# Optimization experiments

Measured on AMD Instinct MI355X. Metric: run time of the kernel, lower is better.

## Reference

```python
import jax, jax.numpy as jnp
import numpy as np

DIM = 1024
HEADS = 16
MLP = 4096
EPS = 1e-5

def _layer_norm(x, g, b):
    mu = jnp.mean(x, axis=-1, keepdims=True)
    var = jnp.mean(jnp.square(x - mu), axis=-1, keepdims=True)
    return (x - mu) * jax.lax.rsqrt(var + EPS) * g + b

def setup_inputs() -> dict:
    key = jax.random.key(0)
    ks = jax.random.split(key, 8)
    s = 0.02
    return {
        "x": jax.random.normal(ks[0], (2, 2048, DIM), dtype=jnp.float32),
        "ln1_g": jnp.ones((DIM,), jnp.float32),
        "ln1_b": jnp.zeros((DIM,), jnp.float32),
        "qkv_w": jax.random.normal(ks[1], (DIM, 3 * DIM), jnp.float32) * s,
        "qkv_b": jnp.zeros((3 * DIM,), jnp.float32),
        "proj_w": jax.random.normal(ks[2], (DIM, DIM), jnp.float32) * s,
        "proj_b": jnp.zeros((DIM,), jnp.float32),
        "ln2_g": jnp.ones((DIM,), jnp.float32),
        "ln2_b": jnp.zeros((DIM,), jnp.float32),
        "fc1_w": jax.random.normal(ks[3], (DIM, MLP), jnp.float32) * s,
        "fc1_b": jnp.zeros((MLP,), jnp.float32),
        "fc2_w": jax.random.normal(ks[4], (MLP, DIM), jnp.float32) * s,
        "fc2_b": jnp.zeros((DIM,), jnp.float32),
    }

def reference(x, ln1_g, ln1_b, qkv_w, qkv_b, proj_w, proj_b,
              ln2_g, ln2_b, fc1_w, fc1_b, fc2_w, fc2_b):
    B, N, C = x.shape
    H = HEADS
    D = C // H
    # --- attention (pre-norm); NOTE: source applies no 1/sqrt(D) scaling ---
    h = _layer_norm(x, ln1_g, ln1_b)
    qkv = (h @ qkv_w + qkv_b).reshape(B, N, 3, H, D)
    q, k, v = (qkv[:, :, 0], qkv[:, :, 1], qkv[:, :, 2])  # [B,N,H,D]
    qk = jnp.einsum('bnhd,bmhd->bhnm', q, k)
    attn = jax.nn.softmax(qk, axis=-1)
    y = jnp.einsum('bhnm,bmhd->bnhd', attn, v).reshape(B, N, C)
    y = y @ proj_w + proj_b
    x = x + y
    # --- MLP (pre-norm), exact GELU like torch nn.GELU ---
    h2 = _layer_norm(x, ln2_g, ln2_b)
    h2 = jax.nn.gelu(h2 @ fc1_w + fc1_b, approximate=False)
    x = x + (h2 @ fc2_w + fc2_b)
    return x
```

## Files before the change

### kernel.cpp

```cpp
#include <hip/hip_runtime.h>
#include <hip/hip_bf16.h>

#define CDIM   1024
#define NSEQ   2048
#define NHEAD  16
#define HDIM   64
#define MLPDIM 4096
#define TROWS  4096

typedef __attribute__((ext_vector_type(8)))  __bf16 bf16x8;
typedef __attribute__((ext_vector_type(4)))  float  f32x4;
typedef __attribute__((ext_vector_type(16))) float  f32x16;
typedef __attribute__((ext_vector_type(4)))  unsigned short us4;

static __device__ __forceinline__ unsigned short f2bf(float f) {
  unsigned int u = __float_as_uint(f);
  u += 0x7fffu + ((u >> 16) & 1u);
  return (unsigned short)(u >> 16);
}

#define MFMA16(a, b, c) __builtin_amdgcn_mfma_f32_16x16x32_bf16(a, b, c, 0, 0, 0)
#define MFMA32(a, b, c) __builtin_amdgcn_mfma_f32_32x32x16_bf16(a, b, c, 0, 0, 0)

static __device__ __forceinline__ void gll16(const unsigned short* g, unsigned short* l) {
  __builtin_amdgcn_global_load_lds(
      (const __attribute__((address_space(1))) unsigned int*)g,
      (__attribute__((address_space(3))) unsigned int*)l, 16, 0, 0);
}

__global__ __launch_bounds__(256)
void ln_bf16_kernel(const float* __restrict__ x,
                    const float* __restrict__ gam,
                    const float* __restrict__ bet,
                    unsigned short* __restrict__ out)
{
  int row = blockIdx.x;
  int t = threadIdx.x;
  const float4* xr = (const float4*)(x + (size_t)row * CDIM);
  float4 v = xr[t];
  float s  = v.x + v.y + v.z + v.w;
  float s2 = v.x*v.x + v.y*v.y + v.z*v.z + v.w*v.w;
  #pragma unroll
  for (int off = 32; off > 0; off >>= 1) {
    s  += __shfl_down(s, off);
    s2 += __shfl_down(s2, off);
  }
  __shared__ float rs[4], rs2[4];
  int wave = t >> 6, lane = t & 63;
  if (lane == 0) { rs[wave] = s; rs2[wave] = s2; }
  __syncthreads();
  float fs  = rs[0] + rs[1] + rs[2] + rs[3];
  float fs2 = rs2[0] + rs2[1] + rs2[2] + rs2[3];
  float mu   = fs * (1.0f / CDIM);
  float var  = fs2 * (1.0f / CDIM) - mu * mu;
  float rstd = rsqrtf(var + 1e-5f);
  float4 gg = ((const float4*)gam)[t];
  float4 bb = ((const float4*)bet)[t];
  us4 o;
  o.x = f2bf((v.x - mu) * rstd * gg.x + bb.x);
  o.y = f2bf((v.y - mu) * rstd * gg.y + bb.y);
  o.z = f2bf((v.z - mu) * rstd * gg.z + bb.z);
  o.w = f2bf((v.w - mu) * rstd * gg.w + bb.w);
  ((us4*)(out + (size_t)row * CDIM))[t] = o;
}

__global__ __launch_bounds__(256)
void ln_add_bf16_kernel(float* __restrict__ x, const float* __restrict__ pp,
                        const float* __restrict__ gam, const float* __restrict__ bet,
                        unsigned short* __restrict__ out)
{
  int row = blockIdx.x;
  int t = threadIdx.x;
  float4* xr = (float4*)(x + (size_t)row * CDIM);
  const float4* pr = (const float4*)(pp + (size_t)row * CDIM);
  float4 v = xr[t];
  float4 q = pr[t];
  v.x += q.x; v.y += q.y; v.z += q.z; v.w += q.w;
  xr[t] = v;
  float s  = v.x + v.y + v.z + v.w;
  float s2 = v.x*v.x + v.y*v.y + v.z*v.z + v.w*v.w;
  #pragma unroll
  for (int off = 32; off > 0; off >>= 1) {
    s  += __shfl_down(s, off);
    s2 += __shfl_down(s2, off);
  }
  __shared__ float rs[4], rs2[4];
  int wave = t >> 6, lane = t & 63;
  if (lane == 0) { rs[wave] = s; rs2[wave] = s2; }
  __syncthreads();
  float fs  = rs[0] + rs[1] + rs[2] + rs[3];
  float fs2 = rs2[0] + rs2[1] + rs2[2] + rs2[3];
  float mu   = fs * (1.0f / CDIM);
  float var  = fs2 * (1.0f / CDIM) - mu * mu;
  float rstd = rsqrtf(var + 1e-5f);
  float4 gg = ((const float4*)gam)[t];
  float4 bb = ((const float4*)bet)[t];
  us4 o;
  o.x = f2bf((v.x - mu) * rstd * gg.x + bb.x);
  o.y = f2bf((v.y - mu) * rstd * gg.y + bb.y);
  o.z = f2bf((v.z - mu) * rstd * gg.z + bb.z);
  o.w = f2bf((v.w - mu) * rstd * gg.w + bb.w);
  ((us4*)(out + (size_t)row * CDIM))[t] = o;
}

__global__ __launch_bounds__(256)
void wt_bf16_kernel(const float* __restrict__ W, unsigned short* __restrict__ Wt,
                    int K, int N)
{
  __shared__ float tile[32][33];
  int n0 = blockIdx.x * 32, k0 = blockIdx.y * 32;
  int t = threadIdx.x;
  int r = t >> 3, c4 = (t & 7) << 2;
  float4 v = *(const float4*)(W + (size_t)(k0 + r) * N + n0 + c4);
  tile[r][c4 + 0] = v.x; tile[r][c4 + 1] = v.y;
  tile[r][c4 + 2] = v.z; tile[r][c4 + 3] = v.w;
  __syncthreads();
  us4 o;
  o.x = f2bf(tile[c4 + 0][r]);
  o.y = f2bf(tile[c4 + 1][r]);
  o.z = f2bf(tile[c4 + 2][r]);
  o.w = f2bf(tile[c4 + 3][r]);
  *(us4*)(Wt + (size_t)(n0 + r) * K + k0 + c4) = o;
}

template<int EPI>
__global__ __launch_bounds__(256, 4)
void gemm_bt(const unsigned short* __restrict__ A, const unsigned short* __restrict__ Bt,
             const float* __restrict__ bias, int Kstride, int Kc, int nbx, int nby,
             float* __restrict__ outf, unsigned short* __restrict__ outb,
             const float* __restrict__ resid, float* __restrict__ pp,
             unsigned short* __restrict__ qo, unsigned short* __restrict__ ko,
             unsigned short* __restrict__ vo)
{
  __shared__ unsigned short As[2][128 * 32];
  __shared__ unsigned short Bs[2][128 * 32];
  const int tid  = threadIdx.x;
  const int lane = tid & 63;
  const int wave = tid >> 6;
  const int wr = wave >> 1, wc = wave & 1;
  const int g = lane >> 4, r16 = lane & 15;

  const int nwg = gridDim.x;
  const int orig = ((int)blockIdx.x & 7) * (nwg >> 3) + ((int)blockIdx.x >> 3);
  const int bx = orig % nbx;
  const int t2 = orig / nbx;
  const int by = t2 % nby;
  const int kz = t2 / nby;
  const int bm = by * 128, bn = bx * 128;
  const int kbase = kz * Kc;
  const int N = nbx * 128;

  auto stage = [&](int d, int k0) {
    #pragma unroll
    for (int c = 0; c < 2; c++) {
      int o   = (c * 256 + tid) << 3;
      int row = o >> 5;
      int col = o & 31;
      int ub  = (c * 256 + (tid & ~63)) << 3;
      gll16(A  + (size_t)(bm + row) * Kstride + kbase + k0 + col, &As[d][ub]);
      gll16(Bt + (size_t)(bn + row) * Kstride + kbase + k0 + col, &Bs[d][ub]);
    }
  };

  f32x4 acc[4][4];
  #pragma unroll
  for (int i = 0; i < 4; i++)
    #pragma unroll
    for (int j = 0; j < 4; j++) acc[i][j] = (f32x4){0.f, 0.f, 0.f, 0.f};

  stage(0, 0);
  const int nkt = Kc / 32;
  for (int kt = 0; kt < nkt; kt++) {
    const int cur = kt & 1;
    __syncthreads();
    if (kt + 1 < nkt) stage(cur ^ 1, (kt + 1) * 32);
    bf16x8 af[4], bfr[4];
    #pragma unroll
    for (int i = 0; i < 4; i++) {
      int row = wr * 64 + i * 16 + r16;
      af[i] = *(const bf16x8*)(&As[cur][row * 32 + 8 * g]);
    }
    #pragma unroll
    for (int j = 0; j < 4; j++) {
      int row = wc * 64 + j * 16 + r16;
      bfr[j] = *(const bf16x8*)(&Bs[cur][row * 32 + 8 * g]);
    }
    __builtin_amdgcn_s_setprio(1);
    #pragma unroll
    for (int i = 0; i < 4; i++)
      #pragma unroll
      for (int j = 0; j < 4; j++)
        acc[i][j] = MFMA16(af[i], bfr[j], acc[i][j]);
    __builtin_amdgcn_s_setprio(0);
  }

  #pragma unroll
  for (int i = 0; i < 4; i++) {
    #pragma unroll
    for (int j = 0; j < 4; j++) {
      int col = bn + wc * 64 + j * 16 + r16;
      float bv = (EPI == 2 && kz != 0) ? 0.f : bias[col];
      #pragma unroll
      for (int jj = 0; jj < 4; jj++) {
        int row = bm + wr * 64 + i * 16 + 4 * g + jj;
        float val = acc[i][j][jj] + bv;
        if (EPI == 1) {
          int sel = col >> 10, cc = col & 1023;
          int hh = cc >> 6, d = cc & 63;
          int b = row >> 11, tk = row & 2047;
          size_t hb = (size_t)(b * NHEAD + hh);
          if (sel == 0)      qo[(hb * NSEQ + tk) * HDIM + d] = f2bf(val * 1.4426950408889634f);
          else if (sel == 1) ko[(hb * NSEQ + tk) * HDIM + d] = f2bf(val);
          else               vo[(hb * HDIM + d) * NSEQ + tk] = f2bf(val);
        } else if (EPI == 2) {
          size_t idx = (size_t)row * N + col;
          if (kz == 0) outf[idx] = val + resid[idx];
          else         pp[idx]   = val;
        } else {
          float vv = val * val;
          float u2 = val * (2.3022361f + 0.1029445f * vv);
          float ge = val - val / (1.0f + exp2f(u2));
          outb[(size_t)row * N + col] = f2bf(ge);
        }
      }
    }
  }
}

__global__ __launch_bounds__(256)
void add_kernel(float* __restrict__ out, const float* __restrict__ pp, int n4)
{
  int i = blockIdx.x * 256 + threadIdx.x;
  int stride = gridDim.x * 256;
  for (; i < n4; i += stride) {
    float4 a = ((const float4*)out)[i];
    float4 b = ((const float4*)pp)[i];
    a.x += b.x; a.y += b.y; a.z += b.z; a.w += b.w;
    ((float4*)out)[i] = a;
  }
}

__global__ __launch_bounds__(256, 4)
void attn_kernel(const unsigned short* __restrict__ q, const unsigned short* __restrict__ k,
                 const unsigned short* __restrict__ vt, unsigned short* __restrict__ y)
{
  int bid = blockIdx.x;
  int xcd = bid & 7, loc = bid >> 3;
  int bh  = xcd * 4 + (loc >> 5);
  int qb64 = loc & 31;
  int b = bh >> 4, h = bh & 15;
  int wave = threadIdx.x >> 6, lane = threadIdx.x & 63;
  int qt = wave >> 1, kvh = wave & 1;
  int ql = lane & 31;
  int hi = lane >> 5;
  int q0 = qb64 * 64 + qt * 32;
  const int kvbase = kvh * (NSEQ / 2);
  const unsigned short* qb = q  + (size_t)bh * NSEQ * HDIM;
  const unsigned short* kb = k  + (size_t)bh * NSEQ * HDIM;
  const unsigned short* vb = vt + (size_t)bh * HDIM * NSEQ;

  __shared__ unsigned short KL[2][2][2048];
  __shared__ unsigned short VL[2][2][2048];

  auto stage = [&](int d, int it) {
    int kv0 = kvbase + it * 32;
    #pragma unroll
    for (int i = 0; i < 2; i++) {
      int c = i * 128 + qt * 64 + lane;
      int row = c >> 3, col = c & 7;
      int sc  = (row << 3) | (col ^ (row & 7));
      gll16(kb + (size_t)kv0 * HDIM + sc * 8, &KL[kvh][d][(i * 128 + qt * 64) * 8]);
    }
    #pragma unroll
    for (int i = 0; i < 2; i++) {
      int c = i * 128 + qt * 64 + lane;
      int row = c >> 2, col = c & 3;
      int scol = col ^ ((row >> 1) & 3);
      gll16(vb + (size_t)row * NSEQ + kv0 + scol * 8, &VL[kvh][d][(i * 128 + qt * 64) * 8]);
    }
  };

  bf16x8 aq[4];
  #pragma unroll
  for (int s = 0; s < 4; s++)
    aq[s] = *(const bf16x8*)(qb + (size_t)(q0 + ql) * HDIM + s * 16 + hi * 8);

  float ssum = 0.f;
  f32x16 o0, o1;
  #pragma unroll
  for (int r = 0; r < 16; r++) { o0[r] = 0.f; o1[r] = 0.f; }

  stage(0, 0);
  const int nit = NSEQ / 64;
  for (int it = 0; it < nit; it++) {
    const int cur = it & 1;
    __syncthreads();
    if (it + 1 < nit) stage(cur ^ 1, it + 1);
    bf16x8 kf[4];
    #pragma unroll
    for (int s = 0; s < 4; s++)
      kf[s] = *(const bf16x8*)((const char*)KL[kvh][cur] +
               ql * 128 + ((((s << 1) | hi) ^ (ql & 7)) << 4));
    f32x16 sacc;
    #pragma unroll
    for (int r = 0; r < 16; r++) sacc[r] = -32.0f;
    __builtin_amdgcn_s_setprio(1);
    #pragma unroll
    for (int s = 0; s < 4; s++)
      sacc = MFMA32(kf[s], aq[s], sacc);
    __builtin_amdgcn_s_setprio(0);
    float ps = 0.f;
    #pragma unroll
    for (int r = 0; r < 16; r++) {
      sacc[r] = exp2f(sacc[r]);
      ps += sacc[r];
    }
    ssum += ps;
    bf16x8 vf[2][2];
    #pragma unroll
    for (int t = 0; t < 2; t++)
      #pragma unroll
      for (int db = 0; db < 2; db++)
        vf[t][db] = *(const bf16x8*)((const char*)VL[kvh][cur] +
                     (db * 32 + ql) * 64 + ((((t << 1) | hi) ^ ((ql >> 1) & 3)) << 4));
    __builtin_amdgcn_s_setprio(1);
    #pragma unroll
    for (int t = 0; t < 2; t++) {
      unsigned pk01, pk23, pk45, pk67;
      asm("v_cvt_pk_bf16_f32 %0, %1, %2" : "=v"(pk01) : "v"(sacc[8*t+0]), "v"(sacc[8*t+1]));
      asm("v_cvt_pk_bf16_f32 %0, %1, %2" : "=v"(pk23) : "v"(sacc[8*t+2]), "v"(sacc[8*t+3]));
      asm("v_cvt_pk_bf16_f32 %0, %1, %2" : "=v"(pk45) : "v"(sacc[8*t+4]), "v"(sacc[8*t+5]));
      asm("v_cvt_pk_bf16_f32 %0, %1, %2" : "=v"(pk67) : "v"(sacc[8*t+6]), "v"(sacc[8*t+7]));
      asm("v_permlane32_swap_b32 %0, %1" : "+v"(pk01), "+v"(pk45));
      asm("v_permlane32_swap_b32 %0, %1" : "+v"(pk23), "+v"(pk67));
      union { unsigned u[4]; bf16x8 v; } pf;
      pf.u[0] = pk01; pf.u[1] = pk23; pf.u[2] = pk45; pf.u[3] = pk67;
      o0 = MFMA32(vf[t][0], pf.v, o0);
      o1 = MFMA32(vf[t][1], pf.v, o1);
    }
    __builtin_amdgcn_s_setprio(0);
  }

  __syncthreads();
  float* OM = (float*)&KL[0][0][0];
  float* SM = (float*)&VL[0][0][0];
  if (kvh == 1) {
    #pragma unroll
    for (int r = 0; r < 16; r++) {
      OM[r * 128 + qt * 64 + lane]        = o0[r];
      OM[(16 + r) * 128 + qt * 64 + lane] = o1[r];
    }
    SM[qt * 64 + lane] = ssum;
  }
  __syncthreads();
  if (kvh == 0) {
    float st = ssum + SM[qt * 64 + lane];
    st += __shfl_xor(st, 32);
    float inv = 1.0f / st;
    #pragma unroll
    for (int r = 0; r < 16; r++) {
      o0[r] += OM[r * 128 + qt * 64 + lane];
      o1[r] += OM[(16 + r) * 128 + qt * 64 + lane];
    }
    unsigned short* yr = y + ((size_t)(b * NSEQ + q0 + ql)) * CDIM + h * HDIM;
    #pragma unroll
    for (int db = 0; db < 2; db++) {
      const f32x16& oo = db ? o1 : o0;
      #pragma unroll
      for (int rq = 0; rq < 4; rq++) {
        us4 w;
        w.x = f2bf(oo[4*rq+0] * inv);
        w.y = f2bf(oo[4*rq+1] * inv);
        w.z = f2bf(oo[4*rq+2] * inv);
        w.w = f2bf(oo[4*rq+3] * inv);
        *(us4*)(yr + db * 32 + rq * 8 + hi * 4) = w;
      }
    }
  }
}

extern "C" void kernel_launch(void* const* d_in, const int* in_sizes, int n_in,
                              void* d_out, int out_size, void* d_ws, size_t ws_size,
                              hipStream_t stream)
{
  const float* x      = (const float*)d_in[0];
  const float* ln1_g  = (const float*)d_in[1];
  const float* ln1_b  = (const float*)d_in[2];
  const float* qkv_w  = (const float*)d_in[3];
  const float* qkv_b  = (const float*)d_in[4];
  const float* proj_w = (const float*)d_in[5];
  const float* proj_b = (const float*)d_in[6];
  const float* ln2_g  = (const float*)d_in[7];
  const float* ln2_b  = (const float*)d_in[8];
  const float* fc1_w  = (const float*)d_in[9];
  const float* fc1_b  = (const float*)d_in[10];
  const float* fc2_w  = (const float*)d_in[11];
  const float* fc2_b  = (const float*)d_in[12];
  float* out = (float*)d_out;

  char* p = (char*)d_ws;
  size_t off = 0;
  auto alloc = [&](size_t bytes) -> void* {
    void* r = p + off; off += (bytes + 255) & ~(size_t)255; return r;
  };
  unsigned short* wt_qkv  = (unsigned short*)alloc((size_t)3072 * 1024 * 2);
  unsigned short* wt_proj = (unsigned short*)alloc((size_t)1024 * 1024 * 2);
  unsigned short* wt_fc1  = (unsigned short*)alloc((size_t)4096 * 1024 * 2);
  unsigned short* wt_fc2  = (unsigned short*)alloc((size_t)1024 * 4096 * 2);
  unsigned short* h1  = (unsigned short*)alloc((size_t)TROWS * CDIM * 2);
  unsigned short* qb  = (unsigned short*)alloc((size_t)TROWS * CDIM * 2);
  unsigned short* kb  = (unsigned short*)alloc((size_t)TROWS * CDIM * 2);
  unsigned short* vtb = (unsigned short*)alloc((size_t)TROWS * CDIM * 2);
  unsigned short* yb  = (unsigned short*)alloc((size_t)TROWS * CDIM * 2);
  float*          x1  = (float*)alloc((size_t)TROWS * CDIM * 4);
  unsigned short* h2  = (unsigned short*)alloc((size_t)TROWS * CDIM * 2);
  unsigned short* g1  = (unsigned short*)alloc((size_t)TROWS * MLPDIM * 2);
  float* pp = (float*)qb;

  dim3 blk(256);
  wt_bf16_kernel<<<dim3(3072 / 32, 1024 / 32), blk, 0, stream>>>(qkv_w, wt_qkv, 1024, 3072);
  wt_bf16_kernel<<<dim3(1024 / 32, 1024 / 32), blk, 0, stream>>>(proj_w, wt_proj, 1024, 1024);
  wt_bf16_kernel<<<dim3(4096 / 32, 1024 / 32), blk, 0, stream>>>(fc1_w, wt_fc1, 1024, 4096);
  wt_bf16_kernel<<<dim3(1024 / 32, 4096 / 32), blk, 0, stream>>>(fc2_w, wt_fc2, 4096, 1024);
  ln_bf16_kernel<<<TROWS, blk, 0, stream>>>(x, ln1_g, ln1_b, h1);
  gemm_bt<1><<<dim3(768), blk, 0, stream>>>(
      h1, wt_qkv, qkv_b, 1024, 1024, 24, 32,
      nullptr, nullptr, nullptr, nullptr, qb, kb, vtb);
  attn_kernel<<<dim3(1024), blk, 0, stream>>>(qb, kb, vtb, yb);
  gemm_bt<2><<<dim3(512), blk, 0, stream>>>(
      yb, wt_proj, proj_b, 1024, 512, 8, 32,
      x1, nullptr, x, pp, nullptr, nullptr, nullptr);
  ln_add_bf16_kernel<<<TROWS, blk, 0, stream>>>(x1, pp, ln2_g, ln2_b, h2);
  gemm_bt<3><<<dim3(1024), blk, 0, stream>>>(
      h2, wt_fc1, fc1_b, 1024, 1024, 32, 32,
      nullptr, g1, nullptr, nullptr, nullptr, nullptr, nullptr);
  gemm_bt<2><<<dim3(512), blk, 0, stream>>>(
      g1, wt_fc2, fc2_b, 4096, 2048, 8, 32,
      out, nullptr, x1, pp, nullptr, nullptr, nullptr);
  add_kernel<<<dim3(2048), blk, 0, stream>>>(out, pp, TROWS * CDIM / 4);
}
```

Baseline: 287.3 us.

## Stage V output through LDS for coalesced transposed stores; double attention KV tile size

```diff
diff --git a/kernel.cpp b/kernel.cpp
--- a/kernel.cpp
+++ b/kernel.cpp
@@ -194,6 +194,36 @@
     __builtin_amdgcn_s_setprio(0);
   }
 
+  if (EPI == 1 && bn >= 2048) {
+    unsigned short* T = (unsigned short*)&As[0][0];
+    __syncthreads();
+    #pragma unroll
+    for (int i = 0; i < 4; i++) {
+      #pragma unroll
+      for (int j = 0; j < 4; j++) {
+        int col_l = wc * 64 + j * 16 + r16;
+        float bv = bias[bn + col_l];
+        #pragma unroll
+        for (int jj = 0; jj < 4; jj++) {
+          int row = wr * 64 + i * 16 + 4 * g + jj;
+          *(unsigned short*)((char*)T + col_l * 256 + ((row * 2) ^ ((col_l & 7) << 4))) =
+              f2bf(acc[i][j][jj] + bv);
+        }
+      }
+    }
+    __syncthreads();
+    int bb = bm >> 11, tk0 = bm & 2047;
+    #pragma unroll
+    for (int c = 0; c < 32; c++) {
+      int col_l = wave * 32 + c;
+      int cv = (bn - 2048) + col_l;
+      int hh = cv >> 6, d = cv & 63;
+      unsigned v2 = *(unsigned*)((char*)T + col_l * 256 + ((lane * 4) ^ ((col_l & 7) << 4)));
+      *(unsigned*)(vo + ((size_t)(bb * NHEAD + hh) * HDIM + d) * NSEQ + tk0 + lane * 2) = v2;
+    }
+    return;
+  }
+
   #pragma unroll
   for (int i = 0; i < 4; i++) {
     #pragma unroll
@@ -205,13 +235,12 @@
         int row = bm + wr * 64 + i * 16 + 4 * g + jj;
         float val = acc[i][j][jj] + bv;
         if (EPI == 1) {
-          int sel = col >> 10, cc = col & 1023;
+          int cc = col & 1023;
           int hh = cc >> 6, d = cc & 63;
           int b = row >> 11, tk = row & 2047;
           size_t hb = (size_t)(b * NHEAD + hh);
-          if (sel == 0)      qo[(hb * NSEQ + tk) * HDIM + d] = f2bf(val * 1.4426950408889634f);
-          else if (sel == 1) ko[(hb * NSEQ + tk) * HDIM + d] = f2bf(val);
-          else               vo[(hb * HDIM + d) * NSEQ + tk] = f2bf(val);
+          if (col < 1024) qo[(hb * NSEQ + tk) * HDIM + d] = f2bf(val * 1.4426950408889634f);
+          else            ko[(hb * NSEQ + tk) * HDIM + d] = f2bf(val);
         } else if (EPI == 2) {
           size_t idx = (size_t)row * N + col;
           if (kz == 0) outf[idx] = val + resid[idx];
@@ -240,7 +269,7 @@
   }
 }
 
-__global__ __launch_bounds__(256, 4)
+__global__ __launch_bounds__(256, 2)
 void attn_kernel(const unsigned short* __restrict__ q, const unsigned short* __restrict__ k,
                  const unsigned short* __restrict__ vt, unsigned short* __restrict__ y)
 {
@@ -259,24 +288,18 @@
   const unsigned short* kb = k  + (size_t)bh * NSEQ * HDIM;
   const unsigned short* vb = vt + (size_t)bh * HDIM * NSEQ;
 
-  __shared__ unsigned short KL[2][2][2048];
-  __shared__ unsigned short VL[2][2][2048];
+  __shared__ unsigned short KL[2][2][4096];
+  __shared__ unsigned short VL[2][2][4096];
 
   auto stage = [&](int d, int it) {
-    int kv0 = kvbase + it * 32;
-    #pragma unroll
-    for (int i = 0; i < 2; i++) {
+    int kv0 = kvbase + it * 64;
+    #pragma unroll
+    for (int i = 0; i < 4; i++) {
       int c = i * 128 + qt * 64 + lane;
       int row = c >> 3, col = c & 7;
-      int sc  = (row << 3) | (col ^ (row & 7));
-      gll16(kb + (size_t)kv0 * HDIM + sc * 8, &KL[kvh][d][(i * 128 + qt * 64) * 8]);
-    }
-    #pragma unroll
-    for (int i = 0; i < 2; i++) {
-      int c = i * 128 + qt * 64 + lane;
-      int row = c >> 2, col = c & 3;
-      int scol = col ^ ((row >> 1) & 3);
-      gll16(vb + (size_t)row * NSEQ + kv0 + scol * 8, &VL[kvh][d][(i * 128 + qt * 64) * 8]);
+      int scol = col ^ (row & 7);
+      gll16(kb + (size_t)(kv0 + row) * HDIM + (scol << 3), &KL[kvh][d][c << 3]);
+      gll16(vb + (size_t)row * NSEQ + kv0 + (scol << 3), &VL[kvh][d][c << 3]);
     }
   };
 
@@ -291,54 +314,63 @@
   for (int r = 0; r < 16; r++) { o0[r] = 0.f; o1[r] = 0.f; }
 
   stage(0, 0);
-  const int nit = NSEQ / 64;
+  const int nit = (NSEQ / 2) / 64;
   for (int it = 0; it < nit; it++) {
     const int cur = it & 1;
     __syncthreads();
     if (it + 1 < nit) stage(cur ^ 1, it + 1);
-    bf16x8 kf[4];
-    #pragma unroll
-    for (int s = 0; s < 4; s++)
-      kf[s] = *(const bf16x8*)((const char*)KL[kvh][cur] +
-               ql * 128 + ((((s << 1) | hi) ^ (ql & 7)) << 4));
-    f32x16 sacc;
-    #pragma unroll
-    for (int r = 0; r < 16; r++) sacc[r] = -32.0f;
-    __builtin_amdgcn_s_setprio(1);
-    #pragma unroll
-    for (int s = 0; s < 4; s++)
-      sacc = MFMA32(kf[s], aq[s], sacc);
-    __builtin_amdgcn_s_setprio(0);
-    float ps = 0.f;
-    #pragma unroll
-    for (int r = 0; r < 16; r++) {
-      sacc[r] = exp2f(sacc[r]);
-      ps += sacc[r];
-    }
-    ssum += ps;
-    bf16x8 vf[2][2];
-    #pragma unroll
-    for (int t = 0; t < 2; t++)
-      #pragma unroll
-      for (int db = 0; db < 2; db++)
-        vf[t][db] = *(const bf16x8*)((const char*)VL[kvh][cur] +
-                     (db * 32 + ql) * 64 + ((((t << 1) | hi) ^ ((ql >> 1) & 3)) << 4));
-    __builtin_amdgcn_s_setprio(1);
-    #pragma unroll
-    for (int t = 0; t < 2; t++) {
-      unsigned pk01, pk23, pk45, pk67;
-      asm("v_cvt_pk_bf16_f32 %0, %1, %2" : "=v"(pk01) : "v"(sacc[8*t+0]), "v"(sacc[8*t+1]));
-      asm("v_cvt_pk_bf16_f32 %0, %1, %2" : "=v"(pk23) : "v"(sacc[8*t+2]), "v"(sacc[8*t+3]));
-      asm("v_cvt_pk_bf16_f32 %0, %1, %2" : "=v"(pk45) : "v"(sacc[8*t+4]), "v"(sacc[8*t+5]));
-      asm("v_cvt_pk_bf16_f32 %0, %1, %2" : "=v"(pk67) : "v"(sacc[8*t+6]), "v"(sacc[8*t+7]));
-      asm("v_permlane32_swap_b32 %0, %1" : "+v"(pk01), "+v"(pk45));
-      asm("v_permlane32_swap_b32 %0, %1" : "+v"(pk23), "+v"(pk67));
-      union { unsigned u[4]; bf16x8 v; } pf;
-      pf.u[0] = pk01; pf.u[1] = pk23; pf.u[2] = pk45; pf.u[3] = pk67;
-      o0 = MFMA32(vf[t][0], pf.v, o0);
-      o1 = MFMA32(vf[t][1], pf.v, o1);
-    }
-    __builtin_amdgcn_s_setprio(0);
+    #pragma unroll
+    for (int sub = 0; sub < 2; sub++) {
+      bf16x8 kf[4];
+      #pragma unroll
+      for (int s = 0; s < 4; s++) {
+        int row = sub * 32 + ql;
+        int cs = (s << 1) | hi;
+        kf[s] = *(const bf16x8*)((const char*)KL[kvh][cur] +
+                 row * 128 + ((cs ^ (row & 7)) << 4));
+      }
+      f32x16 sacc;
+      #pragma unroll
+      for (int r = 0; r < 16; r++) sacc[r] = -32.0f;
+      __builtin_amdgcn_s_setprio(1);
+      #pragma unroll
+      for (int s = 0; s < 4; s++)
+        sacc = MFMA32(kf[s], aq[s], sacc);
+      __builtin_amdgcn_s_setprio(0);
+      float ps = 0.f;
+      #pragma unroll
+      for (int r = 0; r < 16; r++) {
+        sacc[r] = exp2f(sacc[r]);
+        ps += sacc[r];
+      }
+      ssum += ps;
+      bf16x8 vf[2][2];
+      #pragma unroll
+      for (int t = 0; t < 2; t++)
+        #pragma unroll
+        for (int db = 0; db < 2; db++) {
+          int row = db * 32 + ql;
+          int cv = (sub << 2) | (t << 1) | hi;
+          vf[t][db] = *(const bf16x8*)((const char*)VL[kvh][cur] +
+                       row * 128 + ((cv ^ (row & 7)) << 4));
+        }
+      __builtin_amdgcn_s_setprio(1);
+      #pragma unroll
+      for (int t = 0; t < 2; t++) {
+        unsigned pk01, pk23, pk45, pk67;
+        asm("v_cvt_pk_bf16_f32 %0, %1, %2" : "=v"(pk01) : "v"(sacc[8*t+0]), "v"(sacc[8*t+1]));
+        asm("v_cvt_pk_bf16_f32 %0, %1, %2" : "=v"(pk23) : "v"(sacc[8*t+2]), "v"(sacc[8*t+3]));
+        asm("v_cvt_pk_bf16_f32 %0, %1, %2" : "=v"(pk45) : "v"(sacc[8*t+4]), "v"(sacc[8*t+5]));
+        asm("v_cvt_pk_bf16_f32 %0, %1, %2" : "=v"(pk67) : "v"(sacc[8*t+6]), "v"(sacc[8*t+7]));
+        asm("v_permlane32_swap_b32 %0, %1" : "+v"(pk01), "+v"(pk45));
+        asm("v_permlane32_swap_b32 %0, %1" : "+v"(pk23), "+v"(pk67));
+        union { unsigned u[4]; bf16x8 v; } pf;
+        pf.u[0] = pk01; pf.u[1] = pk23; pf.u[2] = pk45; pf.u[3] = pk67;
+        o0 = MFMA32(vf[t][0], pf.v, o0);
+        o1 = MFMA32(vf[t][1], pf.v, o1);
+      }
+      __builtin_amdgcn_s_setprio(0);
+    }
   }
 
   __syncthreads();
```

Result: no change. 286.6 us (-0.2%).
